# Kernel optimization log

Hardware: AMD Instinct MI355X
Metric: run time of the kernel (lower is better)

Reference implementation:

```python
import jax, jax.numpy as jnp
import numpy as np

D = 128; H = 8; DH = D // H
N = 50000; B = 8; MAXN = N // B
E = 400000
NG_G = 4; NG_L = 4; NG = NG_G + NG_L
DFF = 2 * D


def _ln(x, eps=1e-5):
    m = x.mean(-1, keepdims=True)
    v = ((x - m) ** 2).mean(-1, keepdims=True)
    return (x - m) * jax.lax.rsqrt(v + eps)


def _mha(q, k, v, in_w, in_b, out_w, out_b):
    # torch nn.MultiheadAttention (batch_first, eval) with packed in_proj
    Bq, Lq, d = q.shape; Lk = k.shape[1]
    wq, wk, wv = jnp.split(in_w, 3, axis=0)
    bq, bk, bv = jnp.split(in_b, 3)
    Q = (q @ wq.T + bq).reshape(Bq, Lq, H, DH).transpose(0, 2, 1, 3)
    K = (k @ wk.T + bk).reshape(Bq, Lk, H, DH).transpose(0, 2, 1, 3)
    V = (v @ wv.T + bv).reshape(Bq, Lk, H, DH).transpose(0, 2, 1, 3)
    A = jax.nn.softmax(jnp.einsum('bhqd,bhkd->bhqk', Q, K) / np.float32(np.sqrt(DH)), axis=-1)
    O = jnp.einsum('bhqk,bhkd->bhqd', A, V).transpose(0, 2, 1, 3).reshape(Bq, Lq, d)
    return O @ out_w.T + out_b, A.mean(axis=1)  # averaged attn weights over heads


def _tconv(x, src, dst, Wq, bq, Wk, bk, Wv, bv, Wskip, bskip, Wbeta):
    # PyG TransformerConv(d, d//H, heads=H, beta=True): edge-wise gather-attend-scatter
    n = x.shape[0]
    q = (x @ Wq.T + bq)[dst].reshape(-1, H, DH)   # [E,H,DH] query at target node
    k = (x @ Wk.T + bk)[src].reshape(-1, H, DH)
    v = (x @ Wv.T + bv)[src].reshape(-1, H, DH)
    logits = (q * k).sum(-1) / np.float32(np.sqrt(DH))  # [E,H]
    m = jax.ops.segment_max(logits, dst, num_segments=n)
    m = jnp.where(jnp.isfinite(m), m, 0.0)
    a = jnp.exp(logits - m[dst])
    s = jax.ops.segment_sum(a, dst, num_segments=n)
    alpha = a / (s[dst] + 1e-16)                  # per-target-node softmax (PyG softmax)
    out = jax.ops.segment_sum(v * alpha[..., None], dst, num_segments=n).reshape(n, D)
    xr = x @ Wskip.T + bskip                      # root weight
    beta = jax.nn.sigmoid(jnp.concatenate([out, xr, out - xr], axis=-1) @ Wbeta.T)
    return beta * xr + (1.0 - beta) * out


def setup_inputs() -> dict:
    key = jax.random.key(0)
    ks = jax.random.split(key, 16)
    w = lambda i, shape, s=0.05: jax.random.normal(ks[i], shape, jnp.float32) * s
    return dict(
        x=w(0, (N, D), 1.0),
        edge_index=jax.random.randint(ks[1], (2, E), 0, N),
        global_h=w(2, (B, NG, D), 1.0),
        batch=jnp.repeat(jnp.arange(B, dtype=jnp.int32), MAXN),  # sorted, even split
        n_global_tokens_global=NG_G,
        n_global_tokens_local=NG_L,
        Wq=w(3, (D, D)), bq=jnp.zeros((D,), jnp.float32),
        Wk=w(4, (D, D)), bk=jnp.zeros((D,), jnp.float32),
        Wv=w(5, (D, D)), bv=jnp.zeros((D,), jnp.float32),
        Wskip=w(6, (D, D)), bskip=jnp.zeros((D,), jnp.float32),
        Wbeta=w(7, (1, 3 * D)),
        ng_in_w=w(8, (3 * D, D)), ng_in_b=jnp.zeros((3 * D,), jnp.float32),
        ng_out_w=w(9, (D, D)), ng_out_b=jnp.zeros((D,), jnp.float32),
        gn_in_w=w(10, (3 * D, D)), gn_in_b=jnp.zeros((3 * D,), jnp.float32),
        gn_out_w=w(11, (D, D)), gn_out_b=jnp.zeros((D,), jnp.float32),
        W1=w(12, (DFF, D)), b1=jnp.zeros((DFF,), jnp.float32),
        W2=w(13, (D, DFF)), b2=jnp.zeros((D,), jnp.float32),
    )


def reference(x, edge_index, global_h, batch, n_global_tokens_global, n_global_tokens_local,
              Wq, bq, Wk, bk, Wv, bv, Wskip, bskip, Wbeta,
              ng_in_w, ng_in_b, ng_out_w, ng_out_b,
              gn_in_w, gn_in_b, gn_out_w, gn_out_b,
              W1, b1, W2, b2):
    src, dst = edge_index[0], edge_index[1]
    h_local = _tconv(x, src, dst, Wq, bq, Wk, bk, Wv, bv, Wskip, bskip, Wbeta)
    x = _ln(x + h_local)
    Bg = global_h.shape[0]
    # to_dense_batch: batch is sorted with equal-size graphs -> mask all True, pure reshape
    dense_x = x.reshape(Bg, -1, D)
    global_out, attn_w = _mha(global_h, dense_x, dense_x, ng_in_w, ng_in_b, ng_out_w, ng_out_b)
    global_h = _ln(global_h + global_out)
    nodes_out, _ = _mha(dense_x, global_h, global_h, gn_in_w, gn_in_b, gn_out_w, gn_out_b)
    dense_x = _ln(dense_x + nodes_out)
    x = dense_x.reshape(-1, D)  # un-scatter (even split -> reshape)
    ff = jax.nn.relu(x @ W1.T + b1) @ W2.T + b2
    x = _ln(x + ff)
    # attention regularization, vectorized over the per-graph python loop
    ls = n_global_tokens_global
    le = ls + n_global_tokens_local
    P = attn_w[:, ls:le, :]                      # [B, K, max_n], all nodes valid
    Pn = P / (P.sum(-1, keepdims=True) + 1e-8)
    G = jnp.einsum('bkn,bmn->bkm', Pn, Pn)       # [B, K, K]
    Kt = le - ls
    off = (G.sum(axis=(1, 2)) - jnp.einsum('bkk->b', G)) / (Kt * Kt - Kt)
    reg = off.mean()
    return x, global_h, reg
```

## Files before the change

kernel.cpp:

```cpp
#include <hip/hip_runtime.h>
#include <math.h>

#define D 128
#define H 8
#define NGT 8
#define LSTOK 4
#define NCH 4

typedef short bf16x8 __attribute__((ext_vector_type(8)));
typedef float f32x4  __attribute__((ext_vector_type(4)));

__device__ __forceinline__ short f2bf(float f) {
  union { float f; unsigned u; } v; v.f = f;
  unsigned r = v.u + 0x7FFFu + ((v.u >> 16) & 1u);
  return (short)(r >> 16);
}
__device__ __forceinline__ float bf2f(short s) {
  union { unsigned u; float f; } v;
  v.u = ((unsigned)(unsigned short)s) << 16;
  return v.f;
}
__device__ __forceinline__ float4 bf4(bf16x8 v, int lo) {
  return make_float4(bf2f(v[lo]), bf2f(v[lo + 1]), bf2f(v[lo + 2]), bf2f(v[lo + 3]));
}
__device__ __forceinline__ unsigned pk2(float a, float b) {
  return ((unsigned)(unsigned short)f2bf(b) << 16) | (unsigned short)f2bf(a);
}

__device__ __forceinline__ float dot4(float4 a, float4 b) {
  return a.x*b.x + a.y*b.y + a.z*b.z + a.w*b.w;
}
__device__ __forceinline__ float4 scale_madd(float4 a, float sc, float4 v, float p) {
  return make_float4(fmaf(p, v.x, a.x*sc), fmaf(p, v.y, a.y*sc),
                     fmaf(p, v.z, a.z*sc), fmaf(p, v.w, a.w*sc));
}
__device__ __forceinline__ float4 comb4(float4 a, float e1, float4 c, float e2) {
  return make_float4(a.x*e1 + c.x*e2, a.y*e1 + c.y*e2, a.z*e1 + c.z*e2, a.w*e1 + c.w*e2);
}
__device__ __forceinline__ float4 shfl_xor4(float4 v, int off) {
  return make_float4(__shfl_xor(v.x, off), __shfl_xor(v.y, off),
                     __shfl_xor(v.z, off), __shfl_xor(v.w, off));
}

struct CvtArgs {
  const float* s[10];
  short*       d[10];
  int          n[10];
};

__global__ void cvt_weights(CvtArgs a) {
  int which = blockIdx.y;
  const float* s = a.s[which];
  short* d = a.d[which];
  int n = a.n[which];
  int i = (blockIdx.x * 256 + threadIdx.x) * 4;
  if (i + 3 < n) {
    float4 v = *(const float4*)(s + i);
    d[i]     = f2bf(v.x);
    d[i + 1] = f2bf(v.y);
    d[i + 2] = f2bf(v.z);
    d[i + 3] = f2bf(v.w);
  }
}

__global__ void cvt_x(const float* __restrict__ s, short* __restrict__ d, int n) {
  int i = (blockIdx.x * 256 + threadIdx.x) * 8;
  if (i + 7 < n) {
    float4 a = *(const float4*)(s + i);
    float4 b = *(const float4*)(s + i + 4);
    bf16x8 v;
    v[0] = f2bf(a.x); v[1] = f2bf(a.y); v[2] = f2bf(a.z); v[3] = f2bf(a.w);
    v[4] = f2bf(b.x); v[5] = f2bf(b.y); v[6] = f2bf(b.z); v[7] = f2bf(b.w);
    *(bf16x8*)(d + i) = v;
  }
}

__global__ void concat_bias4(const float* __restrict__ b0, const float* __restrict__ b1,
                             const float* __restrict__ b2, const float* __restrict__ b3,
                             float* __restrict__ out) {
  int t = threadIdx.x;
  out[t] = b0[t]; out[128 + t] = b1[t]; out[256 + t] = b2[t]; out[384 + t] = b3[t];
}

#define EPST 72
template<int K>
__global__ void __launch_bounds__(256) gemm_direct(const short* __restrict__ A,
    const short* __restrict__ Wb, const float* __restrict__ bias,
    short* __restrict__ out16, int C16, int s16,
    float* __restrict__ out32, int s32,
    int Nrows, int Ccols, int relu)
{
  __shared__ short eplds[4][64 * EPST];
  const int t = threadIdx.x;
  const int wid = t >> 6, lane = t & 63;
  const int rowBase = blockIdx.x * 128 + (wid >> 1) * 64;
  const int colBase = blockIdx.y * 128 + (wid & 1) * 64;
  const int lrow = lane & 15;
  const int lk = (lane >> 4) * 8;

  f32x4 acc[4][4];
  f32x4 z4 = {0.f, 0.f, 0.f, 0.f};
#pragma unroll
  for (int m = 0; m < 4; m++)
#pragma unroll
    for (int n = 0; n < 4; n++) acc[m][n] = z4;

  const short* ap[4];
#pragma unroll
  for (int m = 0; m < 4; ++m) {
    int ar = rowBase + m * 16 + lrow;
    if (ar >= Nrows) ar = Nrows - 1;
    ap[m] = A + (size_t)ar * K + lk;
  }
  const short* wp[4];
#pragma unroll
  for (int n = 0; n < 4; ++n)
    wp[n] = Wb + (size_t)(colBase + n * 16 + lrow) * K + lk;

#pragma unroll
  for (int kb = 0; kb < K; kb += 32) {
    bf16x8 af[4], bfr[4];
#pragma unroll
    for (int m = 0; m < 4; ++m) af[m] = *(const bf16x8*)(ap[m] + kb);
#pragma unroll
    for (int n = 0; n < 4; ++n) bfr[n] = *(const bf16x8*)(wp[n] + kb);
#pragma unroll
    for (int m = 0; m < 4; ++m)
#pragma unroll
      for (int n = 0; n < 4; ++n)
        acc[m][n] = __builtin_amdgcn_mfma_f32_16x16x32_bf16(af[m], bfr[n], acc[m][n], 0, 0, 0);
  }

  const int ccol = lane & 15;
  const int rquad = (lane >> 4) * 4;
  if (colBase < C16) {
    short* lds = eplds[wid];
#pragma unroll
    for (int n = 0; n < 4; ++n) {
      float bb = bias[colBase + n * 16 + ccol];
      int col = n * 16 + ccol;
#pragma unroll
      for (int m = 0; m < 4; ++m) {
        int r0 = m * 16 + rquad;
#pragma unroll
        for (int r = 0; r < 4; ++r) {
          float v = acc[m][n][r] + bb;
          if (relu) v = fmaxf(v, 0.f);
          lds[(r0 + r) * EPST + col] = f2bf(v);
        }
      }
    }
    const int jr = lane >> 3, jc = lane & 7;
#pragma unroll
    for (int i = 0; i < 8; ++i) {
      int row = i * 8 + jr;
      int gr = rowBase + row;
      if (gr < Nrows) {
        bf16x8 v = *(const bf16x8*)(lds + row * EPST + jc * 8);
        *(bf16x8*)(out16 + (size_t)gr * s16 + colBase + jc * 8) = v;
      }
    }
  } else {
#pragma unroll
    for (int n = 0; n < 4; ++n) {
      int col = colBase + n * 16 + ccol;
      float bb = bias[col];
#pragma unroll
      for (int m = 0; m < 4; ++m) {
        int row0 = rowBase + m * 16 + rquad;
#pragma unroll
        for (int r = 0; r < 4; ++r) {
          int gr = row0 + r;
          if (gr < Nrows) {
            float v = acc[m][n][r] + bb;
            if (relu) v = fmaxf(v, 0.f);
            out32[(size_t)gr * s32 + (col - C16)] = v;
          }
        }
      }
    }
  }
}

#define FFST 264
__global__ void __launch_bounds__(256) gemm_ff(const short* __restrict__ A,
    const short* __restrict__ W1b, const float* __restrict__ b1,
    const short* __restrict__ W2b, const float* __restrict__ b2,
    float* __restrict__ out, int Nrows)
{
  __shared__ short flds[128 * FFST];
  const int t = threadIdx.x;
  const int wid = t >> 6, lane = t & 63;
  const int rowL = (wid >> 1) * 64;
  const int rowBase = blockIdx.x * 128 + rowL;
  const int lrow = lane & 15;
  const int lk = (lane >> 4) * 8;
  const int ccol = lane & 15;
  const int rquad = (lane >> 4) * 4;
  f32x4 z4 = {0.f, 0.f, 0.f, 0.f};

  const short* ap[4];
#pragma unroll
  for (int m = 0; m < 4; ++m) {
    int ar = rowBase + m * 16 + lrow;
    if (ar >= Nrows) ar = Nrows - 1;
    ap[m] = A + (size_t)ar * 128 + lk;
  }

  for (int cb = 0; cb < 2; ++cb) {
    int colBase = cb * 128 + (wid & 1) * 64;
    f32x4 acc[4][4];
#pragma unroll
    for (int m = 0; m < 4; m++)
#pragma unroll
      for (int n = 0; n < 4; n++) acc[m][n] = z4;
    const short* wp[4];
#pragma unroll
    for (int n = 0; n < 4; ++n)
      wp[n] = W1b + (size_t)(colBase + n * 16 + lrow) * 128 + lk;
#pragma unroll
    for (int kb = 0; kb < 128; kb += 32) {
      bf16x8 af[4], bfr[4];
#pragma unroll
      for (int m = 0; m < 4; ++m) af[m] = *(const bf16x8*)(ap[m] + kb);
#pragma unroll
      for (int n = 0; n < 4; ++n) bfr[n] = *(const bf16x8*)(wp[n] + kb);
#pragma unroll
      for (int m = 0; m < 4; ++m)
#pragma unroll
        for (int n = 0; n < 4; ++n)
          acc[m][n] = __builtin_amdgcn_mfma_f32_16x16x32_bf16(af[m], bfr[n], acc[m][n], 0, 0, 0);
    }
#pragma unroll
    for (int n = 0; n < 4; ++n) {
      int col = colBase + n * 16 + ccol;
      float bb = b1[col];
#pragma unroll
      for (int m = 0; m < 4; ++m) {
        int r0 = rowL + m * 16 + rquad;
#pragma unroll
        for (int r = 0; r < 4; ++r) {
          float v = fmaxf(acc[m][n][r] + bb, 0.f);
          flds[(r0 + r) * FFST + col] = f2bf(v);
        }
      }
    }
  }
  __syncthreads();

  {
    int colBase = (wid & 1) * 64;
    f32x4 acc[4][4];
#pragma unroll
    for (int m = 0; m < 4; m++)
#pragma unroll
      for (int n = 0; n < 4; n++) acc[m][n] = z4;
    const short* wp[4];
#pragma unroll
    for (int n = 0; n < 4; ++n)
      wp[n] = W2b + (size_t)(colBase + n * 16 + lrow) * 256 + lk;
#pragma unroll
    for (int kb = 0; kb < 256; kb += 32) {
      bf16x8 af[4], bfr[4];
#pragma unroll
      for (int m = 0; m < 4; ++m)
        af[m] = *(const bf16x8*)(flds + (rowL + m * 16 + lrow) * FFST + kb + lk);
#pragma unroll
      for (int n = 0; n < 4; ++n) bfr[n] = *(const bf16x8*)(wp[n] + kb);
#pragma unroll
      for (int m = 0; m < 4; ++m)
#pragma unroll
        for (int n = 0; n < 4; ++n)
          acc[m][n] = __builtin_amdgcn_mfma_f32_16x16x32_bf16(af[m], bfr[n], acc[m][n], 0, 0, 0);
    }
#pragma unroll
    for (int n = 0; n < 4; ++n) {
      int col = colBase + n * 16 + ccol;
      float bb = b2[col];
#pragma unroll
      for (int m = 0; m < 4; ++m) {
        int row0 = rowBase + m * 16 + rquad;
#pragma unroll
        for (int r = 0; r < 4; ++r) {
          int gr = row0 + r;
          if (gr < Nrows) out[(size_t)gr * 128 + col] = acc[m][n][r] + bb;
        }
      }
    }
  }
}

__global__ void gemm_small(const float* __restrict__ A, const float* __restrict__ W,
                           const float* __restrict__ bias, float* __restrict__ out, int M)
{
  int r = blockIdx.x;
  int c = threadIdx.x;
  __shared__ float as[128];
  as[c] = A[(size_t)r * 128 + c];
  __syncthreads();
  float acc = bias[c];
  const float* wr = W + (size_t)c * 128;
#pragma unroll 4
  for (int k = 0; k < 128; k++) acc += as[k] * wr[k];
  out[(size_t)r * 128 + c] = acc;
}

__global__ void count_deg(const int* __restrict__ dst, int* __restrict__ deg, int E) {
  int e = blockIdx.x * 256 + threadIdx.x;
  if (e < E) atomicAdd(&deg[dst[e]], 1);
}

__global__ void scan_pass1(const int* __restrict__ deg, int* __restrict__ bsum, int N) {
  int t = threadIdx.x, lane = t & 63, wid = t >> 6;
  int idx = blockIdx.x * 1024 + t * 4;
  int4 v = {0, 0, 0, 0};
  if (idx + 3 < N) v = *(const int4*)(deg + idx);
  else {
    if (idx < N) v.x = deg[idx];
    if (idx + 1 < N) v.y = deg[idx + 1];
    if (idx + 2 < N) v.z = deg[idx + 2];
    if (idx + 3 < N) v.w = deg[idx + 3];
  }
  int s = v.x + v.y + v.z + v.w;
#pragma unroll
  for (int off = 32; off >= 1; off >>= 1) s += __shfl_xor(s, off);
  __shared__ int ws[4];
  if (lane == 0) ws[wid] = s;
  __syncthreads();
  if (t == 0) bsum[blockIdx.x] = ws[0] + ws[1] + ws[2] + ws[3];
}

__global__ void scan_pass2(int* __restrict__ bsum, int SB) {
  __shared__ int sh[1024];
  int t = threadIdx.x;
  sh[t] = (t < SB) ? bsum[t] : 0;
  __syncthreads();
  for (int off = 1; off < 1024; off <<= 1) {
    int v = (t >= off) ? sh[t - off] : 0;
    __syncthreads();
    sh[t] += v;
    __syncthreads();
  }
  if (t < SB) bsum[t] = (t == 0) ? 0 : sh[t - 1];
}

__global__ void scan_pass3(const int* __restrict__ deg, const int* __restrict__ bsum,
                           int* __restrict__ row_start, int* __restrict__ cursor,
                           int N, int E)
{
  int t = threadIdx.x, lane = t & 63, wid = t >> 6;
  int idx = blockIdx.x * 1024 + t * 4;
  int4 v = {0, 0, 0, 0};
  if (idx + 3 < N) v = *(const int4*)(deg + idx);
  else {
    if (idx < N) v.x = deg[idx];
    if (idx + 1 < N) v.y = deg[idx + 1];
    if (idx + 2 < N) v.z = deg[idx + 2];
    if (idx + 3 < N) v.w = deg[idx + 3];
  }
  int ts = v.x + v.y + v.z + v.w;
  int x = ts;
#pragma unroll
  for (int off = 1; off < 64; off <<= 1) {
    int y = __shfl_up(x, off);
    if (lane >= off) x += y;
  }
  __shared__ int ws[4];
  if (lane == 63) ws[wid] = x;
  __syncthreads();
  int woff = 0;
  for (int i = 0; i < wid; i++) woff += ws[i];
  int p = bsum[blockIdx.x] + woff + (x - ts);
  if (idx < N)     { row_start[idx] = p; cursor[idx] = p; }     p += v.x;
  if (idx + 1 < N) { row_start[idx + 1] = p; cursor[idx + 1] = p; } p += v.y;
  if (idx + 2 < N) { row_start[idx + 2] = p; cursor[idx + 2] = p; } p += v.z;
  if (idx + 3 < N) { row_start[idx + 3] = p; cursor[idx + 3] = p; }
  if (blockIdx.x == 0 && t == 0) row_start[N] = E;
}

__global__ void fill_edges(const int* __restrict__ dst, const int* __restrict__ src,
                           int* __restrict__ cursor, int* __restrict__ edge_src, int E) {
  int e = blockIdx.x * 256 + threadIdx.x;
  if (e < E) {
    int p = atomicAdd(&cursor[dst[e]], 1);
    edge_src[p] = src[e];
  }
}

__global__ void tconv_attn(const short* __restrict__ qkvb,
                           const int* __restrict__ row_start,
                           const int* __restrict__ edge_src,
                           float* __restrict__ out, int N)
{
  int gid = blockIdx.x * 256 + threadIdx.x;
  if (gid >= N * H) return;
  int n = gid >> 3, h = gid & 7;
  const short* qp = qkvb + (size_t)n * 512 + h * 16;
  bf16x8 qa = *(const bf16x8*)(qp);
  bf16x8 qb = *(const bf16x8*)(qp + 8);
  float4 q0 = bf4(qa, 0), q1 = bf4(qa, 4), q2 = bf4(qb, 0), q3 = bf4(qb, 4);
  int e0 = row_start[n], e1 = row_start[n + 1];

  float mA = -3.0e38f, sA = 0.f;
  float4 A0 = make_float4(0, 0, 0, 0), A1 = A0, A2 = A0, A3 = A0;
  float mB = -3.0e38f, sB = 0.f;
  float4 B0 = A0, B1 = A0, B2 = A0, B3 = A0;

  int ei = e0;
  for (; ei + 1 < e1; ei += 2) {
    int sn0 = edge_src[ei], sn1 = edge_src[ei + 1];
    const short* kp0 = qkvb + (size_t)sn0 * 512 + 128 + h * 16;
    const short* kp1 = qkvb + (size_t)sn1 * 512 + 128 + h * 16;
    bf16x8 k00 = *(const bf16x8*)(kp0);
    bf16x8 k01 = *(const bf16x8*)(kp0 + 8);
    bf16x8 k10 = *(const bf16x8*)(kp1);
    bf16x8 k11 = *(const bf16x8*)(kp1 + 8);
    float d0 = (dot4(q0, bf4(k00, 0)) + dot4(q1, bf4(k00, 4))
              + dot4(q2, bf4(k01, 0)) + dot4(q3, bf4(k01, 4))) * 0.25f;
    float d1 = (dot4(q0, bf4(k10, 0)) + dot4(q1, bf4(k10, 4))
              + dot4(q2, bf4(k11, 0)) + dot4(q3, bf4(k11, 4))) * 0.25f;
    bf16x8 v00 = *(const bf16x8*)(kp0 + 128);
    bf16x8 v01 = *(const bf16x8*)(kp0 + 136);
    bf16x8 v10 = *(const bf16x8*)(kp1 + 128);
    bf16x8 v11 = *(const bf16x8*)(kp1 + 136);
    float mn0 = fmaxf(mA, d0);
    float sc0 = expf(mA - mn0), p0 = expf(d0 - mn0);
    A0 = scale_madd(A0, sc0, bf4(v00, 0), p0);
    A1 = scale_madd(A1, sc0, bf4(v00, 4), p0);
    A2 = scale_madd(A2, sc0, bf4(v01, 0), p0);
    A3 = scale_madd(A3, sc0, bf4(v01, 4), p0);
    sA = sA * sc0 + p0; mA = mn0;
    float mn1 = fmaxf(mB, d1);
    float sc1 = expf(mB - mn1), p1 = expf(d1 - mn1);
    B0 = scale_madd(B0, sc1, bf4(v10, 0), p1);
    B1 = scale_madd(B1, sc1, bf4(v10, 4), p1);
    B2 = scale_madd(B2, sc1, bf4(v11, 0), p1);
    B3 = scale_madd(B3, sc1, bf4(v11, 4), p1);
    sB = sB * sc1 + p1; mB = mn1;
  }
  if (ei < e1) {
    int sn0 = edge_src[ei];
    const short* kp0 = qkvb + (size_t)sn0 * 512 + 128 + h * 16;
    bf16x8 k00 = *(const bf16x8*)(kp0);
    bf16x8 k01 = *(const bf16x8*)(kp0 + 8);
    float d0 = (dot4(q0, bf4(k00, 0)) + dot4(q1, bf4(k00, 4))
              + dot4(q2, bf4(k01, 0)) + dot4(q3, bf4(k01, 4))) * 0.25f;
    bf16x8 v00 = *(const bf16x8*)(kp0 + 128);
    bf16x8 v01 = *(const bf16x8*)(kp0 + 136);
    float mn0 = fmaxf(mA, d0);
    float sc0 = expf(mA - mn0), p0 = expf(d0 - mn0);
    A0 = scale_madd(A0, sc0, bf4(v00, 0), p0);
    A1 = scale_madd(A1, sc0, bf4(v00, 4), p0);
    A2 = scale_madd(A2, sc0, bf4(v01, 0), p0);
    A3 = scale_madd(A3, sc0, bf4(v01, 4), p0);
    sA = sA * sc0 + p0; mA = mn0;
  }
  float mn = fmaxf(mA, mB);
  float eA = expf(mA - mn), eB = expf(mB - mn);
  float s = sA * eA + sB * eB;
  float4 a0 = comb4(A0, eA, B0, eB);
  float4 a1 = comb4(A1, eA, B1, eB);
  float4 a2 = comb4(A2, eA, B2, eB);
  float4 a3 = comb4(A3, eA, B3, eB);
  float inv = 1.f / (s + 1e-16f);
  float4* o4 = (float4*)(out + (size_t)n * 128 + h * 16);
  o4[0] = make_float4(a0.x * inv, a0.y * inv, a0.z * inv, a0.w * inv);
  o4[1] = make_float4(a1.x * inv, a1.y * inv, a1.z * inv, a1.w * inv);
  o4[2] = make_float4(a2.x * inv, a2.y * inv, a2.z * inv, a2.w * inv);
  o4[3] = make_float4(a3.x * inv, a3.y * inv, a3.z * inv, a3.w * inv);
}

__global__ void gate_ln(const float* __restrict__ x, const float* __restrict__ att,
                        const short* __restrict__ qkvb, const float* __restrict__ Wb,
                        float* __restrict__ x1, short* __restrict__ x1b, int N)
{
  int wid = threadIdx.x >> 6, lane = threadIdx.x & 63;
  int n = blockIdx.x * 4 + wid;
  if (n >= N) return;
  size_t base = (size_t)n * 128 + lane * 2;
  float2 o = *(const float2*)(att + base);
  unsigned ru = *(const unsigned*)(qkvb + (size_t)n * 512 + 384 + lane * 2);
  float2 r = make_float2(bf2f((short)(ru & 0xFFFF)), bf2f((short)(ru >> 16)));
  float2 xv = *(const float2*)(x + base);
  float2 w0 = *(const float2*)(Wb + lane * 2);
  float2 w1 = *(const float2*)(Wb + 128 + lane * 2);
  float2 w2 = *(const float2*)(Wb + 256 + lane * 2);
  float ts = o.x * w0.x + o.y * w0.y + r.x * w1.x + r.y * w1.y
           + (o.x - r.x) * w2.x + (o.y - r.y) * w2.y;
#pragma unroll
  for (int mm = 32; mm >= 1; mm >>= 1) ts += __shfl_xor(ts, mm);
  float beta = 1.f / (1.f + expf(-ts));
  float2 y;
  y.x = xv.x + beta * r.x + (1.f - beta) * o.x;
  y.y = xv.y + beta * r.y + (1.f - beta) * o.y;
  float sm = y.x + y.y;
#pragma unroll
  for (int mm = 32; mm >= 1; mm >>= 1) sm += __shfl_xor(sm, mm);
  float mean = sm * (1.f / 128.f);
  float dx = y.x - mean, dy = y.y - mean;
  float vs = dx * dx + dy * dy;
#pragma unroll
  for (int mm = 32; mm >= 1; mm >>= 1) vs += __shfl_xor(vs, mm);
  float rstd = rsqrtf(vs * (1.f / 128.f) + 1e-5f);
  float ox = dx * rstd, oy = dy * rstd;
  *(float2*)(x1 + base) = make_float2(ox, oy);
  *(unsigned*)(x1b + base) = pk2(ox, oy);
}

__global__ void ln_add(const float* __restrict__ a, const float* __restrict__ b,
                       float* __restrict__ out, short* __restrict__ out16, int R)
{
  int wid = threadIdx.x >> 6, lane = threadIdx.x & 63;
  int r = blockIdx.x * 4 + wid;
  if (r >= R) return;
  size_t base = (size_t)r * 128 + lane * 2;
  float2 av = *(const float2*)(a + base);
  float2 bv = *(const float2*)(b + base);
  float2 y = make_float2(av.x + bv.x, av.y + bv.y);
  float sm = y.x + y.y;
#pragma unroll
  for (int mm = 32; mm >= 1; mm >>= 1) sm += __shfl_xor(sm, mm);
  float mean = sm * (1.f / 128.f);
  float dx = y.x - mean, dy = y.y - mean;
  float vs = dx * dx + dy * dy;
#pragma unroll
  for (int mm = 32; mm >= 1; mm >>= 1) vs += __shfl_xor(vs, mm);
  float rstd = rsqrtf(vs * (1.f / 128.f) + 1e-5f);
  float ox = dx * rstd, oy = dy * rstd;
  *(float2*)(out + base) = make_float2(ox, oy);
  if (out16) *(unsigned*)(out16 + base) = pk2(ox, oy);
}

__global__ void glob_part(const float* __restrict__ Qg, const short* __restrict__ kv,
                          float* __restrict__ Plog,
                          float* __restrict__ pm, float* __restrict__ ps,
                          float* __restrict__ pacc, int MAXN)
{
  int blk = blockIdx.x;
  int ch = blockIdx.y;
  int h = blk & 7, g = (blk >> 3) & 7, b = blk >> 6;
  int lane = threadIdx.x;
  const float4* q4 = (const float4*)(Qg + (size_t)(b * NGT + g) * 128 + h * 16);
  float4 q0 = q4[0], q1 = q4[1], q2 = q4[2], q3 = q4[3];
  int chunk = (MAXN + NCH - 1) / NCH;
  int n0 = ch * chunk;
  int n1 = n0 + chunk; if (n1 > MAXN) n1 = MAXN;
  float* plrow = (g >= LSTOK) ? Plog + (((size_t)(b * 4 + g - LSTOK)) * H + h) * MAXN : nullptr;
  float m = -3.0e38f, s = 0.f;
  float4 a0 = make_float4(0, 0, 0, 0), a1 = a0, a2 = a0, a3 = a0;
  for (int n = n0 + lane; n < n1; n += 64) {
    const short* kp = kv + ((size_t)(b * MAXN + n)) * 256 + h * 16;
    bf16x8 k0 = *(const bf16x8*)(kp);
    bf16x8 k1 = *(const bf16x8*)(kp + 8);
    float d = dot4(q0, bf4(k0, 0)) + dot4(q1, bf4(k0, 4))
            + dot4(q2, bf4(k1, 0)) + dot4(q3, bf4(k1, 4));
    d *= 0.25f;
    if (plrow) plrow[n] = d;
    float mn = fmaxf(m, d);
    float sc = expf(m - mn);
    float p = expf(d - mn);
    bf16x8 v0 = *(const bf16x8*)(kp + 128);
    bf16x8 v1 = *(const bf16x8*)(kp + 136);
    a0 = scale_madd(a0, sc, bf4(v0, 0), p);
    a1 = scale_madd(a1, sc, bf4(v0, 4), p);
    a2 = scale_madd(a2, sc, bf4(v1, 0), p);
    a3 = scale_madd(a3, sc, bf4(v1, 4), p);
    s = s * sc + p;
    m = mn;
  }
#pragma unroll
  for (int off = 32; off >= 1; off >>= 1) {
    float m2 = __shfl_xor(m, off);
    float s2 = __shfl_xor(s, off);
    float4 c0 = shfl_xor4(a0, off), c1 = shfl_xor4(a1, off);
    float4 c2 = shfl_xor4(a2, off), c3 = shfl_xor4(a3, off);
    float mn = fmaxf(m, m2);
    float e1 = expf(m - mn), e2 = expf(m2 - mn);
    s = s * e1 + s2 * e2;
    a0 = comb4(a0, e1, c0, e2);
    a1 = comb4(a1, e1, c1, e2);
    a2 = comb4(a2, e1, c2, e2);
    a3 = comb4(a3, e1, c3, e2);
    m = mn;
  }
  if (lane == 0) {
    int pi = blk * NCH + ch;
    pm[pi] = m; ps[pi] = s;
    float4* pa = (float4*)(pacc + (size_t)pi * 16);
    pa[0] = a0; pa[1] = a1; pa[2] = a2; pa[3] = a3;
  }
}

__global__ void glob_merge(const float* __restrict__ pm, const float* __restrict__ ps,
                           const float* __restrict__ pacc, float* __restrict__ Og,
                           float* __restrict__ m_gl, float* __restrict__ is_gl)
{
  int blk = blockIdx.x;
  int lane = threadIdx.x;
  float m = -3.0e38f;
#pragma unroll
  for (int c = 0; c < NCH; ++c) m = fmaxf(m, pm[blk * NCH + c]);
  float s = 0.f;
#pragma unroll
  for (int c = 0; c < NCH; ++c) s += ps[blk * NCH + c] * expf(pm[blk * NCH + c] - m);
  if (lane < 16) {
    float a = 0.f;
#pragma unroll
    for (int c = 0; c < NCH; ++c)
      a += pacc[(size_t)(blk * NCH + c) * 16 + lane] * expf(pm[blk * NCH + c] - m);
    int h = blk & 7, g = (blk >> 3) & 7, b = blk >> 6;
    Og[(size_t)(b * NGT + g) * 128 + h * 16 + lane] = a / s;
  }
  if (lane == 0) { m_gl[blk] = m; is_gl[blk] = 1.f / s; }
}

__global__ void pker2(const float* __restrict__ Plog,
                      const float* __restrict__ m_gl, const float* __restrict__ is_gl,
                      float* __restrict__ P, int MAXN)
{
  int b = blockIdx.y;
  __shared__ float ms[32], iss[32];
  if (threadIdx.x < 32) {
    int g = threadIdx.x >> 3, h = threadIdx.x & 7;
    ms[threadIdx.x]  = m_gl[(b * NGT + LSTOK + g) * H + h];
    iss[threadIdx.x] = is_gl[(b * NGT + LSTOK + g) * H + h];
  }
  __syncthreads();
  int n = blockIdx.x * 256 + threadIdx.x;
  if (n >= MAXN) return;
#pragma unroll
  for (int g = 0; g < 4; g++) {
    float acc = 0.f;
#pragma unroll
    for (int h = 0; h < H; h++) {
      float l = Plog[(((size_t)(b * 4 + g)) * H + h) * MAXN + n];
      acc += expf(l - ms[g * 8 + h]) * iss[g * 8 + h];
    }
    P[(size_t)(b * 4 + g) * MAXN + n] = acc * 0.125f;
  }
}

__global__ void regk(const float* __restrict__ P, float* __restrict__ offb, int MAXN)
{
  int b = blockIdx.x;
  int t = threadIdx.x;
  float v[10];
#pragma unroll
  for (int i = 0; i < 10; i++) v[i] = 0.f;
  for (int n = t; n < MAXN; n += 256) {
    float p0 = P[(size_t)(b * 4 + 0) * MAXN + n];
    float p1 = P[(size_t)(b * 4 + 1) * MAXN + n];
    float p2 = P[(size_t)(b * 4 + 2) * MAXN + n];
    float p3 = P[(size_t)(b * 4 + 3) * MAXN + n];
    v[0] += p0; v[1] += p1; v[2] += p2; v[3] += p3;
    v[4] += p0 * p1; v[5] += p0 * p2; v[6] += p0 * p3;
    v[7] += p1 * p2; v[8] += p1 * p3; v[9] += p2 * p3;
  }
#pragma unroll
  for (int i = 0; i < 10; i++) {
    float x = v[i];
#pragma unroll
    for (int mm = 32; mm >= 1; mm >>= 1) x += __shfl_xor(x, mm);
    v[i] = x;
  }
  __shared__ float red[4][10];
  int wid = t >> 6, lane = t & 63;
  if (lane == 0)
    for (int i = 0; i < 10; i++) red[wid][i] = v[i];
  __syncthreads();
  if (t == 0) {
    float r[10];
    for (int i = 0; i < 10; i++) r[i] = red[0][i] + red[1][i] + red[2][i] + red[3][i];
    float r0 = r[0] + 1e-8f, r1 = r[1] + 1e-8f, r2 = r[2] + 1e-8f, r3 = r[3] + 1e-8f;
    float off = 2.f * (r[4] / (r0 * r1) + r[5] / (r0 * r2) + r[6] / (r0 * r3)
                     + r[7] / (r1 * r2) + r[8] / (r1 * r3) + r[9] / (r2 * r3));
    offb[b] = off * (1.f / 12.f);
  }
}

__global__ void regfin(const float* __restrict__ offb, float* __restrict__ out) {
  if (threadIdx.x == 0 && blockIdx.x == 0) {
    float s = 0.f;
    for (int i = 0; i < 8; i++) s += offb[i];
    *out = s * (1.f / 8.f);
  }
}

__global__ void node_attn(const short* __restrict__ Qn, const float* __restrict__ Kg,
                          const float* __restrict__ Vg, short* __restrict__ On,
                          int N, int MAXN)
{
  __shared__ float kg[2][NGT * 128];
  __shared__ float vg[2][NGT * 128];
  int n0 = blockIdx.x * 32;
  int b0 = n0 / MAXN;
  int nlast = n0 + 31; if (nlast >= N) nlast = N - 1;
  int bLast = nlast / MAXN;
  int nb = (bLast != b0) ? 2 : 1;
  for (int bi = 0; bi < nb; ++bi) {
    size_t gb = (size_t)((b0 + bi) * NGT) * 128;
    int i = threadIdx.x * 4;
    *(float4*)&kg[bi][i] = *(const float4*)(Kg + gb + i);
    *(float4*)&vg[bi][i] = *(const float4*)(Vg + gb + i);
  }
  __syncthreads();
  int n = n0 + (threadIdx.x >> 3), h = threadIdx.x & 7;
  if (n >= N) return;
  int bi = (n / MAXN) - b0;
  const short* qp = Qn + (size_t)n * 128 + h * 16;
  bf16x8 qa = *(const bf16x8*)(qp);
  bf16x8 qb = *(const bf16x8*)(qp + 8);
  float4 q0 = bf4(qa, 0), q1 = bf4(qa, 4), q2 = bf4(qb, 0), q3 = bf4(qb, 4);
  float l[NGT];
  float mx = -3.0e38f;
#pragma unroll
  for (int tk = 0; tk < NGT; tk++) {
    const float4* k4 = (const float4*)(&kg[bi][tk * 128 + h * 16]);
    float d = dot4(q0, k4[0]) + dot4(q1, k4[1]) + dot4(q2, k4[2]) + dot4(q3, k4[3]);
    l[tk] = d * 0.25f;
    mx = fmaxf(mx, l[tk]);
  }
  float s = 0.f;
#pragma unroll
  for (int tk = 0; tk < NGT; tk++) { l[tk] = expf(l[tk] - mx); s += l[tk]; }
  float inv = 1.f / s;
  float4 a0 = make_float4(0, 0, 0, 0), a1 = a0, a2 = a0, a3 = a0;
#pragma unroll
  for (int tk = 0; tk < NGT; tk++) {
    float p = l[tk] * inv;
    const float4* v4 = (const float4*)(&vg[bi][tk * 128 + h * 16]);
    a0 = scale_madd(a0, 1.f, v4[0], p);
    a1 = scale_madd(a1, 1.f, v4[1], p);
    a2 = scale_madd(a2, 1.f, v4[2], p);
    a3 = scale_madd(a3, 1.f, v4[3], p);
  }
  unsigned* o = (unsigned*)(On + (size_t)n * 128 + h * 16);
  o[0] = pk2(a0.x, a0.y); o[1] = pk2(a0.z, a0.w);
  o[2] = pk2(a1.x, a1.y); o[3] = pk2(a1.z, a1.w);
  o[4] = pk2(a2.x, a2.y); o[5] = pk2(a2.z, a2.w);
  o[6] = pk2(a3.x, a3.y); o[7] = pk2(a3.z, a3.w);
}

extern "C" void kernel_launch(void* const* d_in, const int* in_sizes, int n_in,
                              void* d_out, int out_size, void* d_ws, size_t ws_size,
                              hipStream_t stream)
{
  const float* x     = (const float*)d_in[0];
  const int*   ei    = (const int*)d_in[1];
  const float* gh    = (const float*)d_in[2];
  const float* Wq    = (const float*)d_in[6];
  const float* bqv   = (const float*)d_in[7];
  const float* Wk    = (const float*)d_in[8];
  const float* bkv   = (const float*)d_in[9];
  const float* Wv    = (const float*)d_in[10];
  const float* bvv   = (const float*)d_in[11];
  const float* Wsk   = (const float*)d_in[12];
  const float* bsk   = (const float*)d_in[13];
  const float* Wbeta = (const float*)d_in[14];
  const float* ngw   = (const float*)d_in[15];
  const float* ngb   = (const float*)d_in[16];
  const float* ngow  = (const float*)d_in[17];
  const float* ngob  = (const float*)d_in[18];
  const float* gnw   = (const float*)d_in[19];
  const float* gnb   = (const float*)d_in[20];
  const float* gnow  = (const float*)d_in[21];
  const float* gnob  = (const float*)d_in[22];
  const float* W1    = (const float*)d_in[23];
  const float* b1v   = (const float*)d_in[24];
  const float* W2    = (const float*)d_in[25];
  const float* b2v   = (const float*)d_in[26];

  const int N    = in_sizes[0] / D;
  const int E    = in_sizes[1] / 2;
  const int Bb   = 8;
  const int MAXN = N / Bb;

  const int* srcI = ei;
  const int* dstI = ei + E;

  size_t NF = (size_t)N;
  size_t ND = NF * D;
  float* fw = (float*)d_ws;
  short* qkvb = (short*)fw;
  short* kv16 = qkvb;
  short* Qnb  = qkvb + NF * 256;
  short* Onb  = qkvb + NF * 384;
  float* ff2o = fw + NF * 256;
  float* x1   = fw + NF * 384;
  short* x1b  = (short*)(fw + NF * 512);
  float* misc = fw + NF * 576;
  float* Qg    = misc;
  float* Og    = Qg + 8192;
  float* gout  = Og + 8192;
  float* Kg    = gout + 8192;
  float* Vg    = Kg + 8192;
  float* m_gl  = Vg + 8192;
  float* is_gl = m_gl + 512;
  float* Pbuf  = is_gl + 512;
  float* offb  = Pbuf + (size_t)Bb * 4 * MAXN;
  float* bias512 = offb + 16;
  float* Plog  = bias512 + 512;
  float* pm    = Plog + (size_t)4 * H * Bb * MAXN;
  float* ps    = pm + 512 * NCH;
  float* pacc  = ps + 512 * NCH;
  int* deg       = (int*)(pacc + 512 * NCH * 16);
  int* row_start = deg + N;
  int* cursor    = row_start + N + 1;
  int* bsum      = cursor + N;
  int* edge_src  = bsum + 1024;
  short* wbase = (short*)((((uintptr_t)(edge_src + E)) + 15) & ~(uintptr_t)15);
  short* cWq  = wbase;
  short* cWk  = cWq  + 16384;
  short* cWv  = cWk  + 16384;
  short* cWsk = cWv  + 16384;
  short* cNgK = cWsk + 16384;
  short* cNgV = cNgK + 16384;
  short* cGnQ = cNgV + 16384;
  short* cGnO = cGnQ + 16384;
  short* cW1  = cGnO + 16384;
  short* cW2  = cW1  + 32768;
  short* xb   = cW2  + 32768;

  float* outx   = (float*)d_out;
  float* outgh  = outx + ND;
  float* outreg = outgh + (size_t)Bb * NGT * D;
  float* wa     = outx;

  const int GXM = (N + 127) / 128;
  const int SB  = (N + 1023) / 1024;
  dim3 blk256(256);

  CvtArgs ca;
  ca.s[0] = Wq;   ca.d[0] = cWq;  ca.n[0] = 16384;
  ca.s[1] = Wk;   ca.d[1] = cWk;  ca.n[1] = 16384;
  ca.s[2] = Wv;   ca.d[2] = cWv;  ca.n[2] = 16384;
  ca.s[3] = Wsk;  ca.d[3] = cWsk; ca.n[3] = 16384;
  ca.s[4] = ngw + 128 * 128; ca.d[4] = cNgK; ca.n[4] = 16384;
  ca.s[5] = ngw + 256 * 128; ca.d[5] = cNgV; ca.n[5] = 16384;
  ca.s[6] = gnw;  ca.d[6] = cGnQ; ca.n[6] = 16384;
  ca.s[7] = gnow; ca.d[7] = cGnO; ca.n[7] = 16384;
  ca.s[8] = W1;   ca.d[8] = cW1;  ca.n[8] = 32768;
  ca.s[9] = W2;   ca.d[9] = cW2;  ca.n[9] = 32768;
  cvt_weights<<<dim3(32, 10), blk256, 0, stream>>>(ca);
  concat_bias4<<<dim3(1), dim3(128), 0, stream>>>(bqv, bkv, bvv, bsk, bias512);
  cvt_x<<<dim3((N * 128 / 8 + 255) / 256), blk256, 0, stream>>>(x, xb, N * 128);

  hipMemsetAsync(deg, 0, (size_t)N * sizeof(int), stream);
  count_deg<<<dim3((E + 255) / 256), blk256, 0, stream>>>(dstI, deg, E);
  scan_pass1<<<dim3(SB), blk256, 0, stream>>>(deg, bsum, N);
  scan_pass2<<<dim3(1), dim3(1024), 0, stream>>>(bsum, SB);
  scan_pass3<<<dim3(SB), blk256, 0, stream>>>(deg, bsum, row_start, cursor, N, E);
  fill_edges<<<dim3((E + 255) / 256), blk256, 0, stream>>>(dstI, srcI, cursor, edge_src, E);

  gemm_direct<128><<<dim3(GXM, 4), blk256, 0, stream>>>(xb, cWq, bias512,
                                                        qkvb, 512, 512, nullptr, 0,
                                                        N, 512, 0);

  tconv_attn<<<dim3((N * H + 255) / 256), blk256, 0, stream>>>(qkvb, row_start, edge_src, wa, N);
  gate_ln<<<dim3((N + 3) / 4), blk256, 0, stream>>>(x, wa, qkvb, Wbeta, x1, x1b, N);

  gemm_direct<128><<<dim3(GXM, 2), blk256, 0, stream>>>(x1b, cNgK, ngb + 128,
                                                        kv16, 256, 256, nullptr, 0,
                                                        N, 256, 0);
  gemm_small<<<dim3(64), dim3(128), 0, stream>>>(gh, ngw, ngb, Qg, 64);
  glob_part<<<dim3(512, NCH), dim3(64), 0, stream>>>(Qg, kv16, Plog, pm, ps, pacc, MAXN);
  glob_merge<<<dim3(512), dim3(64), 0, stream>>>(pm, ps, pacc, Og, m_gl, is_gl);
  pker2<<<dim3((MAXN + 255) / 256, 8), blk256, 0, stream>>>(Plog, m_gl, is_gl, Pbuf, MAXN);
  regk<<<dim3(8), blk256, 0, stream>>>(Pbuf, offb, MAXN);
  regfin<<<dim3(1), dim3(64), 0, stream>>>(offb, outreg);

  gemm_small<<<dim3(64), dim3(128), 0, stream>>>(Og, ngow, ngob, gout, 64);
  ln_add<<<dim3(16), blk256, 0, stream>>>(gh, gout, outgh, nullptr, 64);

  gemm_small<<<dim3(64), dim3(128), 0, stream>>>(outgh, gnw + 128 * 128, gnb + 128, Kg, 64);
  gemm_small<<<dim3(64), dim3(128), 0, stream>>>(outgh, gnw + 256 * 128, gnb + 256, Vg, 64);
  gemm_direct<128><<<dim3(GXM, 1), blk256, 0, stream>>>(x1b, cGnQ, gnb,
                                                        Qnb, 128, 128, nullptr, 0,
                                                        N, 128, 0);
  node_attn<<<dim3((N + 31) / 32), blk256, 0, stream>>>(Qnb, Kg, Vg, Onb, N, MAXN);
  gemm_direct<128><<<dim3(GXM, 1), blk256, 0, stream>>>(Onb, cGnO, gnob,
                                                        nullptr, 0, 0, wa, 128,
                                                        N, 128, 0);
  ln_add<<<dim3((N + 3) / 4), blk256, 0, stream>>>(x1, wa, x1, x1b, N);

  gemm_ff<<<dim3(GXM), blk256, 0, stream>>>(x1b, cW1, b1v, cW2, b2v, ff2o, N);
  ln_add<<<dim3((N + 3) / 4), blk256, 0, stream>>>(x1, ff2o, outx, nullptr, N);
}
```

Baseline: 367.4 us.

## Fuse x bf16 conversion into QKV GEMM, shrink LDS tiles, store logits bf16

Drops the separate cvt_x kernel and converts fp32 x to bf16 inside the QKV GEMM's A-operand loads, so the bf16 copy of x is never written or re-read. The GEMM epilogue LDS staging is halved by writing out in two 32-row halves. gemm_ff now uses 64-row blocks with half the LDS, giving more blocks and likely better occupancy. The attention logits buffer Plog is stored as bf16, halving its traffic at the cost of some precision in the regularization term.

After: 385.8 us. +5.0%, slower.

```diff
diff --git a/kernel.cpp b/kernel.cpp
--- a/kernel.cpp
+++ b/kernel.cpp
@@ -63,18 +63,6 @@
   }
 }
 
-__global__ void cvt_x(const float* __restrict__ s, short* __restrict__ d, int n) {
-  int i = (blockIdx.x * 256 + threadIdx.x) * 8;
-  if (i + 7 < n) {
-    float4 a = *(const float4*)(s + i);
-    float4 b = *(const float4*)(s + i + 4);
-    bf16x8 v;
-    v[0] = f2bf(a.x); v[1] = f2bf(a.y); v[2] = f2bf(a.z); v[3] = f2bf(a.w);
-    v[4] = f2bf(b.x); v[5] = f2bf(b.y); v[6] = f2bf(b.z); v[7] = f2bf(b.w);
-    *(bf16x8*)(d + i) = v;
-  }
-}
-
 __global__ void concat_bias4(const float* __restrict__ b0, const float* __restrict__ b1,
                              const float* __restrict__ b2, const float* __restrict__ b3,
                              float* __restrict__ out) {
@@ -83,14 +71,14 @@
 }
 
 #define EPST 72
-template<int K>
-__global__ void __launch_bounds__(256) gemm_direct(const short* __restrict__ A,
+template<int K, int AF32>
+__global__ void __launch_bounds__(256) gemm_direct(const void* __restrict__ A,
     const short* __restrict__ Wb, const float* __restrict__ bias,
     short* __restrict__ out16, int C16, int s16,
     float* __restrict__ out32, int s32,
     int Nrows, int Ccols, int relu)
 {
-  __shared__ short eplds[4][64 * EPST];
+  __shared__ short eplds[4][32 * EPST];
   const int t = threadIdx.x;
   const int wid = t >> 6, lane = t & 63;
   const int rowBase = blockIdx.x * 128 + (wid >> 1) * 64;
@@ -105,23 +93,37 @@
 #pragma unroll
     for (int n = 0; n < 4; n++) acc[m][n] = z4;
 
-  const short* ap[4];
+  size_t aidx[4];
 #pragma unroll
   for (int m = 0; m < 4; ++m) {
     int ar = rowBase + m * 16 + lrow;
     if (ar >= Nrows) ar = Nrows - 1;
-    ap[m] = A + (size_t)ar * K + lk;
+    aidx[m] = (size_t)ar * K + lk;
   }
   const short* wp[4];
 #pragma unroll
   for (int n = 0; n < 4; ++n)
     wp[n] = Wb + (size_t)(colBase + n * 16 + lrow) * K + lk;
 
+  const short* A16 = (const short*)A;
+  const float* A32 = (const float*)A;
+
 #pragma unroll
   for (int kb = 0; kb < K; kb += 32) {
     bf16x8 af[4], bfr[4];
 #pragma unroll
-    for (int m = 0; m < 4; ++m) af[m] = *(const bf16x8*)(ap[m] + kb);
+    for (int m = 0; m < 4; ++m) {
+      if (AF32) {
+        float4 f0 = *(const float4*)(A32 + aidx[m] + kb);
+        float4 f1 = *(const float4*)(A32 + aidx[m] + kb + 4);
+        bf16x8 v;
+        v[0] = f2bf(f0.x); v[1] = f2bf(f0.y); v[2] = f2bf(f0.z); v[3] = f2bf(f0.w);
+        v[4] = f2bf(f1.x); v[5] = f2bf(f1.y); v[6] = f2bf(f1.z); v[7] = f2bf(f1.w);
+        af[m] = v;
+      } else {
+        af[m] = *(const bf16x8*)(A16 + aidx[m] + kb);
+      }
+    }
 #pragma unroll
     for (int n = 0; n < 4; ++n) bfr[n] = *(const bf16x8*)(wp[n] + kb);
 #pragma unroll
@@ -135,29 +137,35 @@
   const int rquad = (lane >> 4) * 4;
   if (colBase < C16) {
     short* lds = eplds[wid];
-#pragma unroll
-    for (int n = 0; n < 4; ++n) {
-      float bb = bias[colBase + n * 16 + ccol];
-      int col = n * 16 + ccol;
-#pragma unroll
-      for (int m = 0; m < 4; ++m) {
-        int r0 = m * 16 + rquad;
-#pragma unroll
-        for (int r = 0; r < 4; ++r) {
-          float v = acc[m][n][r] + bb;
-          if (relu) v = fmaxf(v, 0.f);
-          lds[(r0 + r) * EPST + col] = f2bf(v);
+    float bb[4];
+#pragma unroll
+    for (int n = 0; n < 4; ++n) bb[n] = bias[colBase + n * 16 + ccol];
+#pragma unroll
+    for (int half = 0; half < 2; ++half) {
+#pragma unroll
+      for (int n = 0; n < 4; ++n) {
+        int col = n * 16 + ccol;
+#pragma unroll
+        for (int mm = 0; mm < 2; ++mm) {
+          int m = half * 2 + mm;
+          int r0 = mm * 16 + rquad;
+#pragma unroll
+          for (int r = 0; r < 4; ++r) {
+            float v = acc[m][n][r] + bb[n];
+            if (relu) v = fmaxf(v, 0.f);
+            lds[(r0 + r) * EPST + col] = f2bf(v);
+          }
         }
       }
-    }
-    const int jr = lane >> 3, jc = lane & 7;
-#pragma unroll
-    for (int i = 0; i < 8; ++i) {
-      int row = i * 8 + jr;
-      int gr = rowBase + row;
-      if (gr < Nrows) {
-        bf16x8 v = *(const bf16x8*)(lds + row * EPST + jc * 8);
-        *(bf16x8*)(out16 + (size_t)gr * s16 + colBase + jc * 8) = v;
+      const int jr = lane >> 3, jc = lane & 7;
+#pragma unroll
+      for (int i = 0; i < 4; ++i) {
+        int row = i * 8 + jr;
+        int gr = rowBase + half * 32 + row;
+        if (gr < Nrows) {
+          bf16x8 v = *(const bf16x8*)(lds + row * EPST + jc * 8);
+          *(bf16x8*)(out16 + (size_t)gr * s16 + colBase + jc * 8) = v;
+        }
       }
     }
   } else {
@@ -188,27 +196,26 @@
     const short* __restrict__ W2b, const float* __restrict__ b2,
     float* __restrict__ out, int Nrows)
 {
-  __shared__ short flds[128 * FFST];
+  __shared__ short flds[64 * FFST];
   const int t = threadIdx.x;
   const int wid = t >> 6, lane = t & 63;
-  const int rowL = (wid >> 1) * 64;
-  const int rowBase = blockIdx.x * 128 + rowL;
+  const int rowBase = blockIdx.x * 64;
   const int lrow = lane & 15;
   const int lk = (lane >> 4) * 8;
   const int ccol = lane & 15;
   const int rquad = (lane >> 4) * 4;
   f32x4 z4 = {0.f, 0.f, 0.f, 0.f};
 
-  const short* ap[4];
+  size_t aidx[4];
 #pragma unroll
   for (int m = 0; m < 4; ++m) {
     int ar = rowBase + m * 16 + lrow;
     if (ar >= Nrows) ar = Nrows - 1;
-    ap[m] = A + (size_t)ar * 128 + lk;
-  }
-
-  for (int cb = 0; cb < 2; ++cb) {
-    int colBase = cb * 128 + (wid & 1) * 64;
+    aidx[m] = (size_t)ar * 128 + lk;
+  }
+
+  {
+    int colBase = wid * 64;
     f32x4 acc[4][4];
 #pragma unroll
     for (int m = 0; m < 4; m++)
@@ -222,7 +229,7 @@
     for (int kb = 0; kb < 128; kb += 32) {
       bf16x8 af[4], bfr[4];
 #pragma unroll
-      for (int m = 0; m < 4; ++m) af[m] = *(const bf16x8*)(ap[m] + kb);
+      for (int m = 0; m < 4; ++m) af[m] = *(const bf16x8*)(A + aidx[m] + kb);
 #pragma unroll
       for (int n = 0; n < 4; ++n) bfr[n] = *(const bf16x8*)(wp[n] + kb);
 #pragma unroll
@@ -237,7 +244,7 @@
       float bb = b1[col];
 #pragma unroll
       for (int m = 0; m < 4; ++m) {
-        int r0 = rowL + m * 16 + rquad;
+        int r0 = m * 16 + rquad;
 #pragma unroll
         for (int r = 0; r < 4; ++r) {
           float v = fmaxf(acc[m][n][r] + bb, 0.f);
@@ -249,10 +256,11 @@
   __syncthreads();
 
   {
+    int rowL = (wid >> 1) * 32;
     int colBase = (wid & 1) * 64;
-    f32x4 acc[4][4];
-#pragma unroll
-    for (int m = 0; m < 4; m++)
+    f32x4 acc[2][4];
+#pragma unroll
+    for (int m = 0; m < 2; m++)
 #pragma unroll
       for (int n = 0; n < 4; n++) acc[m][n] = z4;
     const short* wp[4];
@@ -261,14 +269,14 @@
       wp[n] = W2b + (size_t)(colBase + n * 16 + lrow) * 256 + lk;
 #pragma unroll
     for (int kb = 0; kb < 256; kb += 32) {
-      bf16x8 af[4], bfr[4];
-#pragma unroll
-      for (int m = 0; m < 4; ++m)
+      bf16x8 af[2], bfr[4];
+#pragma unroll
+      for (int m = 0; m < 2; ++m)
         af[m] = *(const bf16x8*)(flds + (rowL + m * 16 + lrow) * FFST + kb + lk);
 #pragma unroll
       for (int n = 0; n < 4; ++n) bfr[n] = *(const bf16x8*)(wp[n] + kb);
 #pragma unroll
-      for (int m = 0; m < 4; ++m)
+      for (int m = 0; m < 2; ++m)
 #pragma unroll
         for (int n = 0; n < 4; ++n)
           acc[m][n] = __builtin_amdgcn_mfma_f32_16x16x32_bf16(af[m], bfr[n], acc[m][n], 0, 0, 0);
@@ -278,8 +286,8 @@
       int col = colBase + n * 16 + ccol;
       float bb = b2[col];
 #pragma unroll
-      for (int m = 0; m < 4; ++m) {
-        int row0 = rowBase + m * 16 + rquad;
+      for (int m = 0; m < 2; ++m) {
+        int row0 = rowBase + rowL + m * 16 + rquad;
 #pragma unroll
         for (int r = 0; r < 4; ++r) {
           int gr = row0 + r;
@@ -532,7 +540,7 @@
 }
 
 __global__ void glob_part(const float* __restrict__ Qg, const short* __restrict__ kv,
-                          float* __restrict__ Plog,
+                          short* __restrict__ Plog,
                           float* __restrict__ pm, float* __restrict__ ps,
                           float* __restrict__ pacc, int MAXN)
 {
@@ -545,7 +553,7 @@
   int chunk = (MAXN + NCH - 1) / NCH;
   int n0 = ch * chunk;
   int n1 = n0 + chunk; if (n1 > MAXN) n1 = MAXN;
-  float* plrow = (g >= LSTOK) ? Plog + (((size_t)(b * 4 + g - LSTOK)) * H + h) * MAXN : nullptr;
+  short* plrow = (g >= LSTOK) ? Plog + (((size_t)(b * 4 + g - LSTOK)) * H + h) * MAXN : nullptr;
   float m = -3.0e38f, s = 0.f;
   float4 a0 = make_float4(0, 0, 0, 0), a1 = a0, a2 = a0, a3 = a0;
   for (int n = n0 + lane; n < n1; n += 64) {
@@ -555,7 +563,7 @@
     float d = dot4(q0, bf4(k0, 0)) + dot4(q1, bf4(k0, 4))
             + dot4(q2, bf4(k1, 0)) + dot4(q3, bf4(k1, 4));
     d *= 0.25f;
-    if (plrow) plrow[n] = d;
+    if (plrow) plrow[n] = f2bf(d);
     float mn = fmaxf(m, d);
     float sc = expf(m - mn);
     float p = expf(d - mn);
@@ -614,7 +622,7 @@
   if (lane == 0) { m_gl[blk] = m; is_gl[blk] = 1.f / s; }
 }
 
-__global__ void pker2(const float* __restrict__ Plog,
+__global__ void pker2(const short* __restrict__ Plog,
                       const float* __restrict__ m_gl, const float* __restrict__ is_gl,
                       float* __restrict__ P, int MAXN)
 {
@@ -633,7 +641,7 @@
     float acc = 0.f;
 #pragma unroll
     for (int h = 0; h < H; h++) {
-      float l = Plog[(((size_t)(b * 4 + g)) * H + h) * MAXN + n];
+      float l = bf2f(Plog[(((size_t)(b * 4 + g)) * H + h) * MAXN + n]);
       acc += expf(l - ms[g * 8 + h]) * iss[g * 8 + h];
     }
     P[(size_t)(b * 4 + g) * MAXN + n] = acc * 0.125f;
@@ -799,8 +807,8 @@
   float* Pbuf  = is_gl + 512;
   float* offb  = Pbuf + (size_t)Bb * 4 * MAXN;
   float* bias512 = offb + 16;
-  float* Plog  = bias512 + 512;
-  float* pm    = Plog + (size_t)4 * H * Bb * MAXN;
+  short* Plog  = (short*)(bias512 + 512);
+  float* pm    = (float*)(Plog + (size_t)4 * H * Bb * MAXN) + 64;
   float* ps    = pm + 512 * NCH;
   float* pacc  = ps + 512 * NCH;
   int* deg       = (int*)(pacc + 512 * NCH * 16);
@@ -819,7 +827,6 @@
   short* cGnO = cGnQ + 16384;
   short* cW1  = cGnO + 16384;
   short* cW2  = cW1  + 32768;
-  short* xb   = cW2  + 32768;
 
   float* outx   = (float*)d_out;
   float* outgh  = outx + ND;
@@ -843,7 +850,6 @@
   ca.s[9] = W2;   ca.d[9] = cW2;  ca.n[9] = 32768;
   cvt_weights<<<dim3(32, 10), blk256, 0, stream>>>(ca);
   concat_bias4<<<dim3(1), dim3(128), 0, stream>>>(bqv, bkv, bvv, bsk, bias512);
-  cvt_x<<<dim3((N * 128 / 8 + 255) / 256), blk256, 0, stream>>>(x, xb, N * 128);
 
   hipMemsetAsync(deg, 0, (size_t)N * sizeof(int), stream);
   count_deg<<<dim3((E + 255) / 256), blk256, 0, stream>>>(dstI, deg, E);
@@ -852,16 +858,16 @@
   scan_pass3<<<dim3(SB), blk256, 0, stream>>>(deg, bsum, row_start, cursor, N, E);
   fill_edges<<<dim3((E + 255) / 256), blk256, 0, stream>>>(dstI, srcI, cursor, edge_src, E);
 
-  gemm_direct<128><<<dim3(GXM, 4), blk256, 0, stream>>>(xb, cWq, bias512,
-                                                        qkvb, 512, 512, nullptr, 0,
-                                                        N, 512, 0);
+  gemm_direct<128, 1><<<dim3(GXM, 4), blk256, 0, stream>>>(x, cWq, bias512,
+                                                           qkvb, 512, 512, nullptr, 0,
+                                                           N, 512, 0);
 
   tconv_attn<<<dim3((N * H + 255) / 256), blk256, 0, stream>>>(qkvb, row_start, edge_src, wa, N);
   gate_ln<<<dim3((N + 3) / 4), blk256, 0, stream>>>(x, wa, qkvb, Wbeta, x1, x1b, N);
 
-  gemm_direct<128><<<dim3(GXM, 2), blk256, 0, stream>>>(x1b, cNgK, ngb + 128,
-                                                        kv16, 256, 256, nullptr, 0,
-                                                        N, 256, 0);
+  gemm_direct<128, 0><<<dim3(GXM, 2), blk256, 0, stream>>>(x1b, cNgK, ngb + 128,
+                                                           kv16, 256, 256, nullptr, 0,
+                                                           N, 256, 0);
   gemm_small<<<dim3(64), dim3(128), 0, stream>>>(gh, ngw, ngb, Qg, 64);
   glob_part<<<dim3(512, NCH), dim3(64), 0, stream>>>(Qg, kv16, Plog, pm, ps, pacc, MAXN);
   glob_merge<<<dim3(512), dim3(64), 0, stream>>>(pm, ps, pacc, Og, m_gl, is_gl);
@@ -874,15 +880,15 @@
 
   gemm_small<<<dim3(64), dim3(128), 0, stream>>>(outgh, gnw + 128 * 128, gnb + 128, Kg, 64);
   gemm_small<<<dim3(64), dim3(128), 0, stream>>>(outgh, gnw + 256 * 128, gnb + 256, Vg, 64);
-  gemm_direct<128><<<dim3(GXM, 1), blk256, 0, stream>>>(x1b, cGnQ, gnb,
-                                                        Qnb, 128, 128, nullptr, 0,
-                                                        N, 128, 0);
+  gemm_direct<128, 0><<<dim3(GXM, 1), blk256, 0, stream>>>(x1b, cGnQ, gnb,
+                                                           Qnb, 128, 128, nullptr, 0,
+                                                           N, 128, 0);
   node_attn<<<dim3((N + 31) / 32), blk256, 0, stream>>>(Qnb, Kg, Vg, Onb, N, MAXN);
-  gemm_direct<128><<<dim3(GXM, 1), blk256, 0, stream>>>(Onb, cGnO, gnob,
-                                                        nullptr, 0, 0, wa, 128,
-                                                        N, 128, 0);
+  gemm_direct<128, 0><<<dim3(GXM, 1), blk256, 0, stream>>>(Onb, cGnO, gnob,
+                                                           nullptr, 0, 0, wa, 128,
+                                                           N, 128, 0);
   ln_add<<<dim3((N + 3) / 4), blk256, 0, stream>>>(x1, wa, x1, x1b, N);
 
-  gemm_ff<<<dim3(GXM), blk256, 0, stream>>>(x1b, cW1, b1v, cW2, b2v, ff2o, N);
+  gemm_ff<<<dim3((N + 63) / 64), blk256, 0, stream>>>(x1b, cW1, b1v, cW2, b2v, ff2o, N);
   ln_add<<<dim3((N + 3) / 4), blk256, 0, stream>>>(x1, ff2o, outx, nullptr, N);
 }
```
